# Performance work log

Measured on AMD Instinct MI355X. Metric: run time of the kernel, lower is better.

Reference implementation:

```python
import jax, jax.numpy as jnp
import numpy as np

B, T, C, H = 2, 2048, 1024, 16
D = C // H  # head_dim = 64


def setup_inputs() -> dict:
    key = jax.random.key(0)
    k1, k2, k3 = jax.random.split(key, 3)
    scale = 0.02
    return {
        "x": jax.random.normal(k1, (B, T, C), dtype=jnp.float32),
        "w_qkv": jax.random.normal(k2, (C, 3 * C), dtype=jnp.float32) * scale,
        "b_qkv": jnp.zeros((3 * C,), dtype=jnp.float32),
        "w_out": jax.random.normal(k3, (C, C), dtype=jnp.float32) * scale,
        "b_out": jnp.zeros((C,), dtype=jnp.float32),
    }


def reference(x, w_qkv, b_qkv, w_out, b_out):
    b, t, c = x.shape
    qkv = x @ w_qkv + b_qkv                       # [b, t, 3c]
    q, k, v = jnp.split(qkv, 3, axis=-1)
    # [b, t, c] -> [b, h, t, d]
    q = q.reshape(b, t, H, D).transpose(0, 2, 1, 3)
    k = k.reshape(b, t, H, D).transpose(0, 2, 1, 3)
    v = v.reshape(b, t, H, D).transpose(0, 2, 1, 3)
    scores = jnp.einsum("bhqd,bhkd->bhqk", q, k) / jnp.sqrt(jnp.asarray(D, dtype=q.dtype))
    causal = jnp.tril(jnp.ones((t, t), dtype=bool))
    scores = jnp.where(causal, scores, jnp.finfo(scores.dtype).min)
    attn = jax.nn.softmax(scores, axis=-1)        # [b, h, q, k]
    out = jnp.einsum("bhqk,bhkd->bhqd", attn, v)  # [b, h, t, d]
    out = out.transpose(0, 2, 1, 3).reshape(b, t, c)
    return out @ w_out + b_out
```

## Files before the change

kernel.cpp:

```cpp
#include <hip/hip_runtime.h>

#define B_ 2
#define T_ 2048
#define C_ 1024
#define H_ 16
#define D_ 64

using bf16x8 = __attribute__((ext_vector_type(8))) short;
using f32x4  = __attribute__((ext_vector_type(4))) float;

static __device__ __forceinline__ short f2bf(float f) {
  unsigned u = __builtin_bit_cast(unsigned, f);
  unsigned r = u + 0x7fffu + ((u >> 16) & 1u);
  return (short)(r >> 16);
}

#define GLD16(gp, lp) __builtin_amdgcn_global_load_lds( \
    (const __attribute__((address_space(1))) void*)(gp), \
    (__attribute__((address_space(3))) void*)(lp), 16, 0, 0)

__global__ __launch_bounds__(256) void cast_f32_bf16(const float* __restrict__ in,
                                                     short* __restrict__ out) {
  int i = blockIdx.x * blockDim.x + threadIdx.x;
  float4 v = ((const float4*)in)[i];
  short4 o;
  o.x = f2bf(v.x); o.y = f2bf(v.y); o.z = f2bf(v.z); o.w = f2bf(v.w);
  ((short4*)out)[i] = o;
}

__global__ __launch_bounds__(256) void transpose_cast(const float* __restrict__ in,
                                                      short* __restrict__ out,
                                                      int R, int N) {
  __shared__ float tile[32][33];
  int bx = blockIdx.x * 32, by = blockIdx.y * 32;
  int tx = threadIdx.x, ty = threadIdx.y;
  #pragma unroll
  for (int j = 0; j < 32; j += 8)
    tile[ty + j][tx] = in[(size_t)(by + ty + j) * N + bx + tx];
  __syncthreads();
  #pragma unroll
  for (int j = 0; j < 32; j += 8)
    out[(size_t)(bx + ty + j) * R + by + tx] = f2bf(tile[tx][ty + j]);
}

__global__ __launch_bounds__(256) void gemm_qkv(const short* __restrict__ A,
                                                const short* __restrict__ Bt,
                                                const float* __restrict__ bias,
                                                short* __restrict__ Qo,
                                                short* __restrict__ Ko,
                                                short* __restrict__ Vo) {
  __shared__ short sA[128 * 32];
  __shared__ short sB[128 * 32];
  const int tid = threadIdx.x;
  const int w = tid >> 6, lane = tid & 63;
  const int wm = w >> 1, wn = w & 1;
  const int g = lane >> 4, r16 = lane & 15;
  const int m0 = blockIdx.x * 128, n0 = blockIdx.y * 128;
  const int lrow = lane >> 2, slot = lane & 3;

  f32x4 acc[4][4] = {};

  for (int k0 = 0; k0 < 1024; k0 += 32) {
    __syncthreads();
    #pragma unroll
    for (int h = 0; h < 2; ++h) {
      int rbase = h * 64 + w * 16;
      int row = rbase + lrow;
      int sw = (row >> 1) & 3;
      GLD16(&A[(size_t)(m0 + row) * 1024 + k0 + ((slot ^ sw) * 8)], &sA[rbase * 32]);
      GLD16(&Bt[(size_t)(n0 + row) * 1024 + k0 + ((slot ^ sw) * 8)], &sB[rbase * 32]);
    }
    __syncthreads();
    bf16x8 af[4], bf[4];
    #pragma unroll
    for (int mi = 0; mi < 4; ++mi) {
      int row = wm * 64 + mi * 16 + r16;
      af[mi] = *(const bf16x8*)&sA[row * 32 + ((g ^ ((row >> 1) & 3)) * 8)];
    }
    #pragma unroll
    for (int ni = 0; ni < 4; ++ni) {
      int row = wn * 64 + ni * 16 + r16;
      bf[ni] = *(const bf16x8*)&sB[row * 32 + ((g ^ ((row >> 1) & 3)) * 8)];
    }
    __builtin_amdgcn_s_setprio(1);
    #pragma unroll
    for (int mi = 0; mi < 4; ++mi)
      #pragma unroll
      for (int ni = 0; ni < 4; ++ni)
        acc[mi][ni] = __builtin_amdgcn_mfma_f32_16x16x32_bf16(af[mi], bf[ni], acc[mi][ni], 0, 0, 0);
    __builtin_amdgcn_s_setprio(0);
  }

  #pragma unroll
  for (int mi = 0; mi < 4; ++mi) {
    #pragma unroll
    for (int ni = 0; ni < 4; ++ni) {
      int n = n0 + wn * 64 + ni * 16 + r16;
      float bv = bias[n];
      int which = n >> 10;
      int c = n & 1023;
      int hh = c >> 6, d = c & 63;
      short* dst = (which == 0) ? Qo : ((which == 1) ? Ko : Vo);
      float sc = (which == 0) ? 0.18033688f : 1.0f;
      #pragma unroll
      for (int rr = 0; rr < 4; ++rr) {
        int m = m0 + wm * 64 + mi * 16 + g * 4 + rr;
        int b = m >> 11, t = m & 2047;
        dst[(size_t)((b * H_ + hh) * T_ + t) * D_ + d] = f2bf((acc[mi][ni][rr] + bv) * sc);
      }
    }
  }
}

__global__ __launch_bounds__(256) void gemm_out(const short* __restrict__ A,
                                                const short* __restrict__ Bt,
                                                const float* __restrict__ bias,
                                                float* __restrict__ Out) {
  __shared__ short sA[128 * 32];
  __shared__ short sB[128 * 32];
  const int tid = threadIdx.x;
  const int w = tid >> 6, lane = tid & 63;
  const int wm = w >> 1, wn = w & 1;
  const int g = lane >> 4, r16 = lane & 15;
  const int m0 = blockIdx.x * 128, n0 = blockIdx.y * 128;
  const int lrow = lane >> 2, slot = lane & 3;

  f32x4 acc[4][4] = {};

  for (int k0 = 0; k0 < 1024; k0 += 32) {
    __syncthreads();
    #pragma unroll
    for (int h = 0; h < 2; ++h) {
      int rbase = h * 64 + w * 16;
      int row = rbase + lrow;
      int sw = (row >> 1) & 3;
      GLD16(&A[(size_t)(m0 + row) * 1024 + k0 + ((slot ^ sw) * 8)], &sA[rbase * 32]);
      GLD16(&Bt[(size_t)(n0 + row) * 1024 + k0 + ((slot ^ sw) * 8)], &sB[rbase * 32]);
    }
    __syncthreads();
    bf16x8 af[4], bf[4];
    #pragma unroll
    for (int mi = 0; mi < 4; ++mi) {
      int row = wm * 64 + mi * 16 + r16;
      af[mi] = *(const bf16x8*)&sA[row * 32 + ((g ^ ((row >> 1) & 3)) * 8)];
    }
    #pragma unroll
    for (int ni = 0; ni < 4; ++ni) {
      int row = wn * 64 + ni * 16 + r16;
      bf[ni] = *(const bf16x8*)&sB[row * 32 + ((g ^ ((row >> 1) & 3)) * 8)];
    }
    __builtin_amdgcn_s_setprio(1);
    #pragma unroll
    for (int mi = 0; mi < 4; ++mi)
      #pragma unroll
      for (int ni = 0; ni < 4; ++ni)
        acc[mi][ni] = __builtin_amdgcn_mfma_f32_16x16x32_bf16(af[mi], bf[ni], acc[mi][ni], 0, 0, 0);
    __builtin_amdgcn_s_setprio(0);
  }

  #pragma unroll
  for (int mi = 0; mi < 4; ++mi) {
    #pragma unroll
    for (int ni = 0; ni < 4; ++ni) {
      int n = n0 + wn * 64 + ni * 16 + r16;
      float bv = bias[n];
      #pragma unroll
      for (int rr = 0; rr < 4; ++rr) {
        int m = m0 + wm * 64 + mi * 16 + g * 4 + rr;
        Out[(size_t)m * 1024 + n] = acc[mi][ni][rr] + bv;
      }
    }
  }
}

__global__ __launch_bounds__(256, 4) void attn_fwd(const short* __restrict__ Q,
                                                   const short* __restrict__ K,
                                                   const short* __restrict__ V,
                                                   short* __restrict__ O) {
  __shared__ short sK[2][64 * 64];
  __shared__ short vT[2][64 * 64];

  const int tid = threadIdx.x;
  const int w = tid >> 6, lane = tid & 63;
  const int g = lane >> 4, r16 = lane & 15;
  const int bh = blockIdx.x;
  const int b = bh >> 4, hh = bh & 15;
  const int qi = 31 - (int)blockIdx.y;
  const int q0 = qi * 64;

  const short* Qh = Q + (size_t)bh * T_ * D_;
  const short* Kh = K + (size_t)bh * T_ * D_;
  const short* Vh = V + (size_t)bh * T_ * D_;

  const int krow_in_wave = lane >> 3;
  const int kslot = lane & 7;
  const int kp = tid & 31;
  const int vd0 = (tid >> 5) * 8;
  const int vchunk = (kp >> 4) * 4 + ((kp & 7) >> 1);
  const int velem  = ((kp >> 3) & 1) * 4 + 2 * (kp & 1);

  const int qrow_a = q0 + w * 16 + r16;
  bf16x8 qf[2];
  qf[0] = *(const bf16x8*)&Qh[(size_t)qrow_a * 64 + g * 8];
  qf[1] = *(const bf16x8*)&Qh[(size_t)qrow_a * 64 + 32 + g * 8];

  f32x4 o[4] = {};
  float m_ = -1e30f, l_ = 0.f;

  const int nkt = qi + 1;

  #pragma unroll
  for (int p = 0; p < 2; ++p) {
    int row = w * 16 + p * 8 + krow_in_wave;
    GLD16(&Kh[(size_t)row * 64 + ((kslot ^ (row & 7)) * 8)], &sK[0][(w * 16 + p * 8) * 64]);
  }
  {
    int4 v0 = *(const int4*)&Vh[(size_t)(2 * kp) * 64 + vd0];
    int4 v1 = *(const int4*)&Vh[(size_t)(2 * kp + 1) * 64 + vd0];
    const short* a0 = (const short*)&v0;
    const short* a1 = (const short*)&v1;
    #pragma unroll
    for (int j = 0; j < 8; ++j) {
      int d = vd0 + j;
      int val = ((int)(unsigned short)a0[j]) | (((int)(unsigned short)a1[j]) << 16);
      *(int*)&vT[0][d * 64 + ((vchunk ^ j) * 8) + velem] = val;
    }
  }
  __syncthreads();

  for (int kt = 0; kt < nkt; ++kt) {
    const int cur = kt & 1, nxt = cur ^ 1;
    const int k0 = kt * 64;
    const bool pf = (kt + 1 < nkt);

    int4 vn0, vn1;
    if (pf) {
      const int k1 = k0 + 64;
      #pragma unroll
      for (int p = 0; p < 2; ++p) {
        int row = w * 16 + p * 8 + krow_in_wave;
        GLD16(&Kh[(size_t)(k1 + row) * 64 + ((kslot ^ (row & 7)) * 8)],
              &sK[nxt][(w * 16 + p * 8) * 64]);
      }
      vn0 = *(const int4*)&Vh[(size_t)(k1 + 2 * kp) * 64 + vd0];
      vn1 = *(const int4*)&Vh[(size_t)(k1 + 2 * kp + 1) * 64 + vd0];
    }

    f32x4 s[4] = {};
    __builtin_amdgcn_s_setprio(1);
    #pragma unroll
    for (int nt = 0; nt < 4; ++nt) {
      const int row = nt * 16 + r16;
      const int sw8 = r16 & 7;
      bf16x8 kf0 = *(const bf16x8*)&sK[cur][row * 64 + ((g ^ sw8) * 8)];
      bf16x8 kf1 = *(const bf16x8*)&sK[cur][row * 64 + (((4 + g) ^ sw8) * 8)];
      s[nt] = __builtin_amdgcn_mfma_f32_16x16x32_bf16(kf0, qf[0], s[nt], 0, 0, 0);
      s[nt] = __builtin_amdgcn_mfma_f32_16x16x32_bf16(kf1, qf[1], s[nt], 0, 0, 0);
    }
    __builtin_amdgcn_s_setprio(0);

    if (kt == nkt - 1) {
      const int qrow = w * 16 + r16;
      #pragma unroll
      for (int nt = 0; nt < 4; ++nt)
        #pragma unroll
        for (int rr = 0; rr < 4; ++rr)
          if (nt * 16 + 4 * g + rr > qrow) s[nt][rr] = -1e30f;
    }
    float pmax = s[0][0];
    #pragma unroll
    for (int nt = 0; nt < 4; ++nt)
      #pragma unroll
      for (int rr = 0; rr < 4; ++rr)
        pmax = fmaxf(pmax, s[nt][rr]);
    pmax = fmaxf(pmax, __shfl_xor(pmax, 16));
    pmax = fmaxf(pmax, __shfl_xor(pmax, 32));
    if (!__all(pmax - m_ <= 8.0f)) {
      float mn = fmaxf(m_, pmax);
      float al = __builtin_amdgcn_exp2f(m_ - mn);
      m_ = mn;
      l_ *= al;
      float av[4];
      #pragma unroll
      for (int rr = 0; rr < 4; ++rr) av[rr] = __shfl(al, 4 * g + rr, 16);
      #pragma unroll
      for (int nt = 0; nt < 4; ++nt)
        #pragma unroll
        for (int rr = 0; rr < 4; ++rr) o[nt][rr] *= av[rr];
    }
    float rs = 0.f;
    #pragma unroll
    for (int nt = 0; nt < 4; ++nt)
      #pragma unroll
      for (int rr = 0; rr < 4; ++rr) {
        float p = __builtin_amdgcn_exp2f(s[nt][rr] - m_);
        s[nt][rr] = p;
        rs += p;
      }
    rs += __shfl_xor(rs, 16);
    rs += __shfl_xor(rs, 32);
    l_ += rs;
    int pk[8];
    #pragma unroll
    for (int nt = 0; nt < 4; ++nt)
      #pragma unroll
      for (int h = 0; h < 2; ++h)
        asm("v_cvt_pk_bf16_f32 %0, %1, %2"
            : "=v"(pk[nt * 2 + h])
            : "v"(s[nt][2 * h]), "v"(s[nt][2 * h + 1]));

    bf16x8 pa[2];
    {
      int4 t0; t0.x = pk[0]; t0.y = pk[1]; t0.z = pk[2]; t0.w = pk[3];
      int4 t1; t1.x = pk[4]; t1.y = pk[5]; t1.z = pk[6]; t1.w = pk[7];
      pa[0] = __builtin_bit_cast(bf16x8, t0);
      pa[1] = __builtin_bit_cast(bf16x8, t1);
    }
    __builtin_amdgcn_s_setprio(1);
    #pragma unroll
    for (int nt = 0; nt < 4; ++nt) {
      const int d = nt * 16 + r16;
      bf16x8 vb0 = *(const bf16x8*)&vT[cur][d * 64 + ((g ^ (d & 7)) * 8)];
      bf16x8 vb1 = *(const bf16x8*)&vT[cur][d * 64 + (((4 + g) ^ (d & 7)) * 8)];
      o[nt] = __builtin_amdgcn_mfma_f32_16x16x32_bf16(pa[0], vb0, o[nt], 0, 0, 0);
      o[nt] = __builtin_amdgcn_mfma_f32_16x16x32_bf16(pa[1], vb1, o[nt], 0, 0, 0);
    }
    __builtin_amdgcn_s_setprio(0);

    if (pf) {
      const short* a0 = (const short*)&vn0;
      const short* a1 = (const short*)&vn1;
      #pragma unroll
      for (int j = 0; j < 8; ++j) {
        int d = vd0 + j;
        int val = ((int)(unsigned short)a0[j]) | (((int)(unsigned short)a1[j]) << 16);
        *(int*)&vT[nxt][d * 64 + ((vchunk ^ j) * 8) + velem] = val;
      }
    }
    __syncthreads();
  }

  float lv[4];
  #pragma unroll
  for (int rr = 0; rr < 4; ++rr) lv[rr] = __shfl(l_, 4 * g + rr, 16);
  #pragma unroll
  for (int nt = 0; nt < 4; ++nt) {
    int d = nt * 16 + r16;
    #pragma unroll
    for (int rr = 0; rr < 4; ++rr) {
      int t = q0 + w * 16 + 4 * g + rr;
      O[(size_t)(b * T_ + t) * C_ + hh * 64 + d] = f2bf(o[nt][rr] / lv[rr]);
    }
  }
}

extern "C" void kernel_launch(void* const* d_in, const int* in_sizes, int n_in,
                              void* d_out, int out_size, void* d_ws, size_t ws_size,
                              hipStream_t stream) {
  const float* x     = (const float*)d_in[0];
  const float* w_qkv = (const float*)d_in[1];
  const float* b_qkv = (const float*)d_in[2];
  const float* w_out = (const float*)d_in[3];
  const float* b_out = (const float*)d_in[4];
  float* out = (float*)d_out;

  char* ws = (char*)d_ws;
  if (ws_size < (size_t)(40u << 20)) return;

  short* xb     = (short*)(ws);
  short* wqkvT  = (short*)(ws + ((size_t)8u << 20));
  short* woutT  = (short*)(ws + ((size_t)14u << 20));
  short* Qb     = (short*)(ws + ((size_t)16u << 20));
  short* Kb     = (short*)(ws + ((size_t)24u << 20));
  short* Vb     = (short*)(ws + ((size_t)32u << 20));
  short* attn_o = xb;

  cast_f32_bf16<<<4096, 256, 0, stream>>>(x, xb);
  transpose_cast<<<dim3(96, 32), dim3(32, 8), 0, stream>>>(w_qkv, wqkvT, 1024, 3072);
  transpose_cast<<<dim3(32, 32), dim3(32, 8), 0, stream>>>(w_out, woutT, 1024, 1024);
  gemm_qkv<<<dim3(32, 24), 256, 0, stream>>>(xb, wqkvT, b_qkv, Qb, Kb, Vb);
  attn_fwd<<<dim3(32, 32), 256, 0, stream>>>(Qb, Kb, Vb, attn_o);
  gemm_out<<<dim3(32, 8), 256, 0, stream>>>(attn_o, woutT, b_out, out);
}
```

Measured before the change: 134.3 us.

## Double GEMM K-tile depth and triple-buffer K in attention with partial waitcnt

Both projection GEMMs now load 64-wide K tiles per iteration instead of 32, using an 8-slot XOR swizzle and issuing two MFMAs per accumulator. This halves the number of barrier and sync rounds per GEMM at the cost of twice the shared memory. The attention kernel triple-buffers K in shared memory, prefetching two tiles ahead. It replaces __syncthreads with explicit vmcnt and lgkmcnt waits plus s_barrier, so the next K load can stay in flight across the barrier. The extra LDS and hand-placed waitcnt raise occupancy and correctness risks if the vmcnt accounting is off.

```diff
diff --git a/kernel.cpp b/kernel.cpp
--- a/kernel.cpp
+++ b/kernel.cpp
@@ -49,45 +49,50 @@
                                                 short* __restrict__ Qo,
                                                 short* __restrict__ Ko,
                                                 short* __restrict__ Vo) {
-  __shared__ short sA[128 * 32];
-  __shared__ short sB[128 * 32];
+  __shared__ short sA[128 * 64];
+  __shared__ short sB[128 * 64];
   const int tid = threadIdx.x;
   const int w = tid >> 6, lane = tid & 63;
   const int wm = w >> 1, wn = w & 1;
   const int g = lane >> 4, r16 = lane & 15;
   const int m0 = blockIdx.x * 128, n0 = blockIdx.y * 128;
-  const int lrow = lane >> 2, slot = lane & 3;
+  const int krow = lane >> 3, kslot = lane & 7;
 
   f32x4 acc[4][4] = {};
 
-  for (int k0 = 0; k0 < 1024; k0 += 32) {
+  for (int k0 = 0; k0 < 1024; k0 += 64) {
     __syncthreads();
     #pragma unroll
-    for (int h = 0; h < 2; ++h) {
-      int rbase = h * 64 + w * 16;
-      int row = rbase + lrow;
-      int sw = (row >> 1) & 3;
-      GLD16(&A[(size_t)(m0 + row) * 1024 + k0 + ((slot ^ sw) * 8)], &sA[rbase * 32]);
-      GLD16(&Bt[(size_t)(n0 + row) * 1024 + k0 + ((slot ^ sw) * 8)], &sB[rbase * 32]);
+    for (int p = 0; p < 4; ++p) {
+      int rbase = w * 32 + p * 8;
+      int row = rbase + krow;
+      GLD16(&A[(size_t)(m0 + row) * 1024 + k0 + ((kslot ^ (row & 7)) * 8)], &sA[rbase * 64]);
+      GLD16(&Bt[(size_t)(n0 + row) * 1024 + k0 + ((kslot ^ (row & 7)) * 8)], &sB[rbase * 64]);
     }
     __syncthreads();
-    bf16x8 af[4], bf[4];
+    bf16x8 af[4][2], bf[4][2];
     #pragma unroll
     for (int mi = 0; mi < 4; ++mi) {
       int row = wm * 64 + mi * 16 + r16;
-      af[mi] = *(const bf16x8*)&sA[row * 32 + ((g ^ ((row >> 1) & 3)) * 8)];
+      #pragma unroll
+      for (int c = 0; c < 2; ++c)
+        af[mi][c] = *(const bf16x8*)&sA[row * 64 + (((c * 4 + g) ^ (row & 7)) * 8)];
     }
     #pragma unroll
     for (int ni = 0; ni < 4; ++ni) {
       int row = wn * 64 + ni * 16 + r16;
-      bf[ni] = *(const bf16x8*)&sB[row * 32 + ((g ^ ((row >> 1) & 3)) * 8)];
+      #pragma unroll
+      for (int c = 0; c < 2; ++c)
+        bf[ni][c] = *(const bf16x8*)&sB[row * 64 + (((c * 4 + g) ^ (row & 7)) * 8)];
     }
     __builtin_amdgcn_s_setprio(1);
     #pragma unroll
     for (int mi = 0; mi < 4; ++mi)
       #pragma unroll
-      for (int ni = 0; ni < 4; ++ni)
-        acc[mi][ni] = __builtin_amdgcn_mfma_f32_16x16x32_bf16(af[mi], bf[ni], acc[mi][ni], 0, 0, 0);
+      for (int ni = 0; ni < 4; ++ni) {
+        acc[mi][ni] = __builtin_amdgcn_mfma_f32_16x16x32_bf16(af[mi][0], bf[ni][0], acc[mi][ni], 0, 0, 0);
+        acc[mi][ni] = __builtin_amdgcn_mfma_f32_16x16x32_bf16(af[mi][1], bf[ni][1], acc[mi][ni], 0, 0, 0);
+      }
     __builtin_amdgcn_s_setprio(0);
   }
 
@@ -116,45 +121,50 @@
                                                 const short* __restrict__ Bt,
                                                 const float* __restrict__ bias,
                                                 float* __restrict__ Out) {
-  __shared__ short sA[128 * 32];
-  __shared__ short sB[128 * 32];
+  __shared__ short sA[128 * 64];
+  __shared__ short sB[128 * 64];
   const int tid = threadIdx.x;
   const int w = tid >> 6, lane = tid & 63;
   const int wm = w >> 1, wn = w & 1;
   const int g = lane >> 4, r16 = lane & 15;
   const int m0 = blockIdx.x * 128, n0 = blockIdx.y * 128;
-  const int lrow = lane >> 2, slot = lane & 3;
+  const int krow = lane >> 3, kslot = lane & 7;
 
   f32x4 acc[4][4] = {};
 
-  for (int k0 = 0; k0 < 1024; k0 += 32) {
+  for (int k0 = 0; k0 < 1024; k0 += 64) {
     __syncthreads();
     #pragma unroll
-    for (int h = 0; h < 2; ++h) {
-      int rbase = h * 64 + w * 16;
-      int row = rbase + lrow;
-      int sw = (row >> 1) & 3;
-      GLD16(&A[(size_t)(m0 + row) * 1024 + k0 + ((slot ^ sw) * 8)], &sA[rbase * 32]);
-      GLD16(&Bt[(size_t)(n0 + row) * 1024 + k0 + ((slot ^ sw) * 8)], &sB[rbase * 32]);
+    for (int p = 0; p < 4; ++p) {
+      int rbase = w * 32 + p * 8;
+      int row = rbase + krow;
+      GLD16(&A[(size_t)(m0 + row) * 1024 + k0 + ((kslot ^ (row & 7)) * 8)], &sA[rbase * 64]);
+      GLD16(&Bt[(size_t)(n0 + row) * 1024 + k0 + ((kslot ^ (row & 7)) * 8)], &sB[rbase * 64]);
     }
     __syncthreads();
-    bf16x8 af[4], bf[4];
+    bf16x8 af[4][2], bf[4][2];
     #pragma unroll
     for (int mi = 0; mi < 4; ++mi) {
       int row = wm * 64 + mi * 16 + r16;
-      af[mi] = *(const bf16x8*)&sA[row * 32 + ((g ^ ((row >> 1) & 3)) * 8)];
+      #pragma unroll
+      for (int c = 0; c < 2; ++c)
+        af[mi][c] = *(const bf16x8*)&sA[row * 64 + (((c * 4 + g) ^ (row & 7)) * 8)];
     }
     #pragma unroll
     for (int ni = 0; ni < 4; ++ni) {
       int row = wn * 64 + ni * 16 + r16;
-      bf[ni] = *(const bf16x8*)&sB[row * 32 + ((g ^ ((row >> 1) & 3)) * 8)];
+      #pragma unroll
+      for (int c = 0; c < 2; ++c)
+        bf[ni][c] = *(const bf16x8*)&sB[row * 64 + (((c * 4 + g) ^ (row & 7)) * 8)];
     }
     __builtin_amdgcn_s_setprio(1);
     #pragma unroll
     for (int mi = 0; mi < 4; ++mi)
       #pragma unroll
-      for (int ni = 0; ni < 4; ++ni)
-        acc[mi][ni] = __builtin_amdgcn_mfma_f32_16x16x32_bf16(af[mi], bf[ni], acc[mi][ni], 0, 0, 0);
+      for (int ni = 0; ni < 4; ++ni) {
+        acc[mi][ni] = __builtin_amdgcn_mfma_f32_16x16x32_bf16(af[mi][0], bf[ni][0], acc[mi][ni], 0, 0, 0);
+        acc[mi][ni] = __builtin_amdgcn_mfma_f32_16x16x32_bf16(af[mi][1], bf[ni][1], acc[mi][ni], 0, 0, 0);
+      }
     __builtin_amdgcn_s_setprio(0);
   }
 
@@ -177,7 +187,7 @@
                                                    const short* __restrict__ K,
                                                    const short* __restrict__ V,
                                                    short* __restrict__ O) {
-  __shared__ short sK[2][64 * 64];
+  __shared__ short sK[3][64 * 64];
   __shared__ short vT[2][64 * 64];
 
   const int tid = threadIdx.x;
@@ -209,14 +219,22 @@
 
   const int nkt = qi + 1;
 
-  #pragma unroll
-  for (int p = 0; p < 2; ++p) {
-    int row = w * 16 + p * 8 + krow_in_wave;
-    GLD16(&Kh[(size_t)row * 64 + ((kslot ^ (row & 7)) * 8)], &sK[0][(w * 16 + p * 8) * 64]);
-  }
   {
     int4 v0 = *(const int4*)&Vh[(size_t)(2 * kp) * 64 + vd0];
     int4 v1 = *(const int4*)&Vh[(size_t)(2 * kp + 1) * 64 + vd0];
+    #pragma unroll
+    for (int p = 0; p < 2; ++p) {
+      int row = w * 16 + p * 8 + krow_in_wave;
+      GLD16(&Kh[(size_t)row * 64 + ((kslot ^ (row & 7)) * 8)], &sK[0][(w * 16 + p * 8) * 64]);
+    }
+    if (nkt > 1) {
+      #pragma unroll
+      for (int p = 0; p < 2; ++p) {
+        int row = w * 16 + p * 8 + krow_in_wave;
+        GLD16(&Kh[(size_t)(64 + row) * 64 + ((kslot ^ (row & 7)) * 8)],
+              &sK[1][(w * 16 + p * 8) * 64]);
+      }
+    }
     const short* a0 = (const short*)&v0;
     const short* a1 = (const short*)&v1;
     #pragma unroll
@@ -225,26 +243,37 @@
       int val = ((int)(unsigned short)a0[j]) | (((int)(unsigned short)a1[j]) << 16);
       *(int*)&vT[0][d * 64 + ((vchunk ^ j) * 8) + velem] = val;
     }
-  }
-  __syncthreads();
+    if (nkt > 1) asm volatile("s_waitcnt vmcnt(2)" ::: "memory");
+    else         asm volatile("s_waitcnt vmcnt(0)" ::: "memory");
+    asm volatile("s_waitcnt lgkmcnt(0)" ::: "memory");
+    __builtin_amdgcn_sched_barrier(0);
+    __builtin_amdgcn_s_barrier();
+    __builtin_amdgcn_sched_barrier(0);
+  }
 
   for (int kt = 0; kt < nkt; ++kt) {
-    const int cur = kt & 1, nxt = cur ^ 1;
-    const int k0 = kt * 64;
-    const bool pf = (kt + 1 < nkt);
+    const int cur3 = kt % 3;
+    const int curv = kt & 1;
+    const bool pf1 = (kt + 1 < nkt);
+    const bool pf2 = (kt + 2 < nkt);
 
     int4 vn0, vn1;
-    if (pf) {
-      const int k1 = k0 + 64;
+    if (pf1) {
+      const int k1 = (kt + 1) * 64;
+      vn0 = *(const int4*)&Vh[(size_t)(k1 + 2 * kp) * 64 + vd0];
+      vn1 = *(const int4*)&Vh[(size_t)(k1 + 2 * kp + 1) * 64 + vd0];
+    }
+    if (pf2) {
+      const int k2 = (kt + 2) * 64;
+      const int nb = (kt + 2) % 3;
       #pragma unroll
       for (int p = 0; p < 2; ++p) {
         int row = w * 16 + p * 8 + krow_in_wave;
-        GLD16(&Kh[(size_t)(k1 + row) * 64 + ((kslot ^ (row & 7)) * 8)],
-              &sK[nxt][(w * 16 + p * 8) * 64]);
-      }
-      vn0 = *(const int4*)&Vh[(size_t)(k1 + 2 * kp) * 64 + vd0];
-      vn1 = *(const int4*)&Vh[(size_t)(k1 + 2 * kp + 1) * 64 + vd0];
-    }
+        GLD16(&Kh[(size_t)(k2 + row) * 64 + ((kslot ^ (row & 7)) * 8)],
+              &sK[nb][(w * 16 + p * 8) * 64]);
+      }
+    }
+    __builtin_amdgcn_sched_barrier(0);
 
     f32x4 s[4] = {};
     __builtin_amdgcn_s_setprio(1);
@@ -252,8 +281,8 @@
     for (int nt = 0; nt < 4; ++nt) {
       const int row = nt * 16 + r16;
       const int sw8 = r16 & 7;
-      bf16x8 kf0 = *(const bf16x8*)&sK[cur][row * 64 + ((g ^ sw8) * 8)];
-      bf16x8 kf1 = *(const bf16x8*)&sK[cur][row * 64 + (((4 + g) ^ sw8) * 8)];
+      bf16x8 kf0 = *(const bf16x8*)&sK[cur3][row * 64 + ((g ^ sw8) * 8)];
+      bf16x8 kf1 = *(const bf16x8*)&sK[cur3][row * 64 + (((4 + g) ^ sw8) * 8)];
       s[nt] = __builtin_amdgcn_mfma_f32_16x16x32_bf16(kf0, qf[0], s[nt], 0, 0, 0);
       s[nt] = __builtin_amdgcn_mfma_f32_16x16x32_bf16(kf1, qf[1], s[nt], 0, 0, 0);
     }
@@ -320,24 +349,29 @@
     #pragma unroll
     for (int nt = 0; nt < 4; ++nt) {
       const int d = nt * 16 + r16;
-      bf16x8 vb0 = *(const bf16x8*)&vT[cur][d * 64 + ((g ^ (d & 7)) * 8)];
-      bf16x8 vb1 = *(const bf16x8*)&vT[cur][d * 64 + (((4 + g) ^ (d & 7)) * 8)];
+      bf16x8 vb0 = *(const bf16x8*)&vT[curv][d * 64 + ((g ^ (d & 7)) * 8)];
+      bf16x8 vb1 = *(const bf16x8*)&vT[curv][d * 64 + (((4 + g) ^ (d & 7)) * 8)];
       o[nt] = __builtin_amdgcn_mfma_f32_16x16x32_bf16(pa[0], vb0, o[nt], 0, 0, 0);
       o[nt] = __builtin_amdgcn_mfma_f32_16x16x32_bf16(pa[1], vb1, o[nt], 0, 0, 0);
     }
     __builtin_amdgcn_s_setprio(0);
 
-    if (pf) {
+    if (pf1) {
       const short* a0 = (const short*)&vn0;
       const short* a1 = (const short*)&vn1;
       #pragma unroll
       for (int j = 0; j < 8; ++j) {
         int d = vd0 + j;
         int val = ((int)(unsigned short)a0[j]) | (((int)(unsigned short)a1[j]) << 16);
-        *(int*)&vT[nxt][d * 64 + ((vchunk ^ j) * 8) + velem] = val;
-      }
-    }
-    __syncthreads();
+        *(int*)&vT[curv ^ 1][d * 64 + ((vchunk ^ j) * 8) + velem] = val;
+      }
+      if (pf2) asm volatile("s_waitcnt vmcnt(2)" ::: "memory");
+      else     asm volatile("s_waitcnt vmcnt(0)" ::: "memory");
+      asm volatile("s_waitcnt lgkmcnt(0)" ::: "memory");
+      __builtin_amdgcn_sched_barrier(0);
+      __builtin_amdgcn_s_barrier();
+      __builtin_amdgcn_sched_barrier(0);
+    }
   }
 
   float lv[4];
```

Measured after the change: 125.1 us. -6.8%, faster.
